# Kernel optimization log

Measured on AMD Instinct MI355X. Metric: run time of the kernel, lower is better.

The kernel has to match this reference:

```python
import jax, jax.numpy as jnp
import numpy as np

A = 5.0  # smoothness parameter


def setup_inputs() -> dict:
    key = jax.random.key(0)
    kx, kw = jax.random.split(key)
    x = jax.random.uniform(kx, (4096, 256), dtype=jnp.float32)
    weight = jax.random.uniform(kw, (256, 256), dtype=jnp.float32)
    return {"x": x, "weight": weight}


def reference(x, weight):
    # inner: [batch, in_features, out_features] broadcast elementwise max
    inner = jnp.maximum(x[..., None], weight[None])
    # smooth min over in_features (dim=-2): -(1/a) * logsumexp(-a * inner)
    smooth = -jax.nn.logsumexp(-A * inner, axis=-2) / A
    # hard min over same dim
    hard = jnp.min(inner, axis=-2)
    # straight-through estimator: forward value = hard, gradient flows via smooth
    return jax.lax.stop_gradient(hard - smooth) + smooth
```

## Files before the change

### kernel.cpp

```cpp
#include <hip/hip_runtime.h>


typedef _Float16 h2 __attribute__((ext_vector_type(2)));

union U4H { uint4 u; h2 h[4]; };

static __device__ __forceinline__ h2 pmin(h2 a, h2 b) {
#if __has_builtin(__builtin_elementwise_min)
    return __builtin_elementwise_min(a, b);
#else
    h2 d; asm("v_pk_min_f16 %0, %1, %2" : "=v"(d) : "v"(a), "v"(b)); return d;
#endif
}
static __device__ __forceinline__ h2 pmax(h2 a, h2 b) {
#if __has_builtin(__builtin_elementwise_max)
    return __builtin_elementwise_max(a, b);
#else
    h2 d; asm("v_pk_max_f16 %0, %1, %2" : "=v"(d) : "v"(a), "v"(b)); return d;
#endif
}

__global__ __launch_bounds__(256, 1)
void SmoothSTEMinMax_kernel(const float* __restrict__ x,
                            const float* __restrict__ w,
                            float* __restrict__ out) {
    __shared__ __align__(16) unsigned char smem[65536];
    unsigned char* xs = smem;
    unsigned char* ws = smem + 32768;

    const int t  = threadIdx.x;
    const int r0 = blockIdx.y * 64;
    const int c0 = blockIdx.x * 64;

    {
        const int i4 = t & 63;
        const int wv = t >> 6;
#pragma unroll
        for (int k = 0; k < 8; ++k) {
            const int rr = (k << 2) + wv;
            const float4 va = *reinterpret_cast<const float4*>(&x[(size_t)(r0 + rr)      * 256 + (i4 << 2)]);
            const float4 vb = *reinterpret_cast<const float4*>(&x[(size_t)(r0 + rr + 32) * 256 + (i4 << 2)]);
            U4H q;
            q.h[0] = h2{(_Float16)va.x, (_Float16)va.y};
            q.h[1] = h2{(_Float16)va.z, (_Float16)va.w};
            q.h[2] = h2{(_Float16)vb.x, (_Float16)vb.y};
            q.h[3] = h2{(_Float16)vb.z, (_Float16)vb.w};
            const int line = rr ^ (i4 & 31);
            *reinterpret_cast<uint4*>(xs + (i4 << 9) + (line << 4)) = q.u;
        }
    }

#pragma unroll
    for (int k = 0; k < 8; ++k) {
        const int flat = k * 256 + t;
        const int p  = flat >> 4;
        const int cq = flat & 15;
        const float4 va = *reinterpret_cast<const float4*>(&w[(size_t)(2 * p)     * 256 + c0 + (cq << 2)]);
        const float4 vb = *reinterpret_cast<const float4*>(&w[(size_t)(2 * p + 1) * 256 + c0 + (cq << 2)]);
        U4H q;
        q.h[0] = h2{(_Float16)va.x, (_Float16)vb.x};
        q.h[1] = h2{(_Float16)va.y, (_Float16)vb.y};
        q.h[2] = h2{(_Float16)va.z, (_Float16)vb.z};
        q.h[3] = h2{(_Float16)va.w, (_Float16)vb.w};
        *reinterpret_cast<uint4*>(ws + p * 256 + (cq << 4)) = q.u;
    }

    __syncthreads();

    const int tr = t >> 4;
    const int tc = t & 15;

    h2 acc[4][4];
    const h2 big = h2{(_Float16)65504.0f, (_Float16)65504.0f};
#pragma unroll
    for (int m = 0; m < 4; ++m)
#pragma unroll
        for (int n = 0; n < 4; ++n) acc[m][n] = big;

#pragma unroll 4
    for (int i4 = 0; i4 < 64; ++i4) {
        const unsigned char* xb = xs + (i4 << 9);
        const int kk = i4 & 31;
        U4H xu0, xu1, wqa, wqb;
        xu0.u = *reinterpret_cast<const uint4*>(xb + ((((tr << 1)    ) ^ kk) << 4));
        xu1.u = *reinterpret_cast<const uint4*>(xb + ((((tr << 1) | 1) ^ kk) << 4));
        const unsigned char* wb = ws + (i4 << 9);
        wqa.u = *reinterpret_cast<const uint4*>(wb       + (tc << 4));
        wqb.u = *reinterpret_cast<const uint4*>(wb + 256 + (tc << 4));

        h2 xA[4] = { xu0.h[0], xu0.h[2], xu1.h[0], xu1.h[2] };
        h2 xB[4] = { xu0.h[1], xu0.h[3], xu1.h[1], xu1.h[3] };
        h2 wA[4] = { wqa.h[0], wqa.h[1], wqa.h[2], wqa.h[3] };
        h2 wB[4] = { wqb.h[0], wqb.h[1], wqb.h[2], wqb.h[3] };

#pragma unroll
        for (int m = 0; m < 4; ++m)
#pragma unroll
            for (int n = 0; n < 4; ++n) {
                acc[m][n] = pmin(acc[m][n], pmax(xA[m], wA[n]));
                acc[m][n] = pmin(acc[m][n], pmax(xB[m], wB[n]));
            }
    }

    const int rowm[4] = { 2 * tr, 2 * tr + 32, 2 * tr + 1, 2 * tr + 33 };
#pragma unroll
    for (int m = 0; m < 4; ++m) {
        float4 o;
        o.x = fminf((float)acc[m][0].x, (float)acc[m][0].y);
        o.y = fminf((float)acc[m][1].x, (float)acc[m][1].y);
        o.z = fminf((float)acc[m][2].x, (float)acc[m][2].y);
        o.w = fminf((float)acc[m][3].x, (float)acc[m][3].y);
        *reinterpret_cast<float4*>(&out[(size_t)(r0 + rowm[m]) * 256 + c0 + (tc << 2)]) = o;
    }
}

extern "C" void kernel_launch(void* const* d_in, const int* in_sizes, int n_in,
                              void* d_out, int out_size, void* d_ws, size_t ws_size,
                              hipStream_t stream) {
    const float* x = (const float*)d_in[0];
    const float* w = (const float*)d_in[1];
    float* out = (float*)d_out;

    const int batch = in_sizes[0] / 256;
    dim3 grid(256 / 64, batch / 64);
    dim3 block(256);
    hipLaunchKernelGGL(SmoothSTEMinMax_kernel, grid, block, 0, stream, x, w, out);
}
```

Baseline: 19.96 us.

## Use 1024-thread blocks with one output column per thread

Each block now runs 1024 threads instead of 256, and each thread computes 4 outputs (one column, four rows) rather than a 4x4 tile. The weight staging is relaid out so each thread reads an 8-byte slice per k-step, and outputs are written as scalar stores. The aim is more latency hiding and more parallel waves per block, at the cost of less register-level reuse: there are more shared-memory loads per min/max operation and stores are no longer vectorized.

```diff
diff --git a/kernel.cpp b/kernel.cpp
--- a/kernel.cpp
+++ b/kernel.cpp
@@ -4,6 +4,7 @@
 typedef _Float16 h2 __attribute__((ext_vector_type(2)));
 
 union U4H { uint4 u; h2 h[4]; };
+union U2H { uint2 u; h2 h[2]; };
 
 static __device__ __forceinline__ h2 pmin(h2 a, h2 b) {
 #if __has_builtin(__builtin_elementwise_min)
@@ -20,7 +21,7 @@
 #endif
 }
 
-__global__ __launch_bounds__(256, 1)
+__global__ __launch_bounds__(1024, 4)
 void SmoothSTEMinMax_kernel(const float* __restrict__ x,
                             const float* __restrict__ w,
                             float* __restrict__ out) {
@@ -36,8 +37,8 @@
         const int i4 = t & 63;
         const int wv = t >> 6;
 #pragma unroll
-        for (int k = 0; k < 8; ++k) {
-            const int rr = (k << 2) + wv;
+        for (int k = 0; k < 2; ++k) {
+            const int rr = (k << 4) + wv;
             const float4 va = *reinterpret_cast<const float4*>(&x[(size_t)(r0 + rr)      * 256 + (i4 << 2)]);
             const float4 vb = *reinterpret_cast<const float4*>(&x[(size_t)(r0 + rr + 32) * 256 + (i4 << 2)]);
             U4H q;
@@ -51,67 +52,54 @@
     }
 
 #pragma unroll
-    for (int k = 0; k < 8; ++k) {
-        const int flat = k * 256 + t;
-        const int p  = flat >> 4;
-        const int cq = flat & 15;
-        const float4 va = *reinterpret_cast<const float4*>(&w[(size_t)(2 * p)     * 256 + c0 + (cq << 2)]);
-        const float4 vb = *reinterpret_cast<const float4*>(&w[(size_t)(2 * p + 1) * 256 + c0 + (cq << 2)]);
-        U4H q;
-        q.h[0] = h2{(_Float16)va.x, (_Float16)vb.x};
-        q.h[1] = h2{(_Float16)va.y, (_Float16)vb.y};
-        q.h[2] = h2{(_Float16)va.z, (_Float16)vb.z};
-        q.h[3] = h2{(_Float16)va.w, (_Float16)vb.w};
-        *reinterpret_cast<uint4*>(ws + p * 256 + (cq << 4)) = q.u;
+    for (int k = 0; k < 4; ++k) {
+        const int flat = (k << 10) + t;
+        const int i4  = (flat >> 6) & 63;
+        const int col = flat & 63;
+        const float f0 = w[(size_t)((i4 << 2) + 0) * 256 + c0 + col];
+        const float f1 = w[(size_t)((i4 << 2) + 1) * 256 + c0 + col];
+        const float f2 = w[(size_t)((i4 << 2) + 2) * 256 + c0 + col];
+        const float f3 = w[(size_t)((i4 << 2) + 3) * 256 + c0 + col];
+        U2H q;
+        q.h[0] = h2{(_Float16)f0, (_Float16)f1};
+        q.h[1] = h2{(_Float16)f2, (_Float16)f3};
+        *reinterpret_cast<uint2*>(ws + (i4 << 9) + (col << 3)) = q.u;
     }
 
     __syncthreads();
 
-    const int tr = t >> 4;
-    const int tc = t & 15;
+    const int tr = t >> 6;
+    const int tc = t & 63;
 
-    h2 acc[4][4];
+    h2 acc0, acc1, acc2, acc3;
     const h2 big = h2{(_Float16)65504.0f, (_Float16)65504.0f};
-#pragma unroll
-    for (int m = 0; m < 4; ++m)
-#pragma unroll
-        for (int n = 0; n < 4; ++n) acc[m][n] = big;
+    acc0 = acc1 = acc2 = acc3 = big;
 
 #pragma unroll 4
     for (int i4 = 0; i4 < 64; ++i4) {
         const unsigned char* xb = xs + (i4 << 9);
         const int kk = i4 & 31;
-        U4H xu0, xu1, wqa, wqb;
+        U4H xu0, xu1; U2H wq;
         xu0.u = *reinterpret_cast<const uint4*>(xb + ((((tr << 1)    ) ^ kk) << 4));
         xu1.u = *reinterpret_cast<const uint4*>(xb + ((((tr << 1) | 1) ^ kk) << 4));
-        const unsigned char* wb = ws + (i4 << 9);
-        wqa.u = *reinterpret_cast<const uint4*>(wb       + (tc << 4));
-        wqb.u = *reinterpret_cast<const uint4*>(wb + 256 + (tc << 4));
+        wq.u  = *reinterpret_cast<const uint2*>(ws + (i4 << 9) + (tc << 3));
 
-        h2 xA[4] = { xu0.h[0], xu0.h[2], xu1.h[0], xu1.h[2] };
-        h2 xB[4] = { xu0.h[1], xu0.h[3], xu1.h[1], xu1.h[3] };
-        h2 wA[4] = { wqa.h[0], wqa.h[1], wqa.h[2], wqa.h[3] };
-        h2 wB[4] = { wqb.h[0], wqb.h[1], wqb.h[2], wqb.h[3] };
-
-#pragma unroll
-        for (int m = 0; m < 4; ++m)
-#pragma unroll
-            for (int n = 0; n < 4; ++n) {
-                acc[m][n] = pmin(acc[m][n], pmax(xA[m], wA[n]));
-                acc[m][n] = pmin(acc[m][n], pmax(xB[m], wB[n]));
-            }
+        const h2 wA = wq.h[0], wB = wq.h[1];
+        acc0 = pmin(acc0, pmax(xu0.h[0], wA)); acc0 = pmin(acc0, pmax(xu0.h[1], wB));
+        acc1 = pmin(acc1, pmax(xu0.h[2], wA)); acc1 = pmin(acc1, pmax(xu0.h[3], wB));
+        acc2 = pmin(acc2, pmax(xu1.h[0], wA)); acc2 = pmin(acc2, pmax(xu1.h[1], wB));
+        acc3 = pmin(acc3, pmax(xu1.h[2], wA)); acc3 = pmin(acc3, pmax(xu1.h[3], wB));
     }
 
     const int rowm[4] = { 2 * tr, 2 * tr + 32, 2 * tr + 1, 2 * tr + 33 };
-#pragma unroll
-    for (int m = 0; m < 4; ++m) {
-        float4 o;
-        o.x = fminf((float)acc[m][0].x, (float)acc[m][0].y);
-        o.y = fminf((float)acc[m][1].x, (float)acc[m][1].y);
-        o.z = fminf((float)acc[m][2].x, (float)acc[m][2].y);
-        o.w = fminf((float)acc[m][3].x, (float)acc[m][3].y);
-        *reinterpret_cast<float4*>(&out[(size_t)(r0 + rowm[m]) * 256 + c0 + (tc << 2)]) = o;
-    }
+    const float o0 = fminf((float)acc0.x, (float)acc0.y);
+    const float o1 = fminf((float)acc1.x, (float)acc1.y);
+    const float o2 = fminf((float)acc2.x, (float)acc2.y);
+    const float o3 = fminf((float)acc3.x, (float)acc3.y);
+    out[(size_t)(r0 + rowm[0]) * 256 + c0 + tc] = o0;
+    out[(size_t)(r0 + rowm[1]) * 256 + c0 + tc] = o1;
+    out[(size_t)(r0 + rowm[2]) * 256 + c0 + tc] = o2;
+    out[(size_t)(r0 + rowm[3]) * 256 + c0 + tc] = o3;
 }
 
 extern "C" void kernel_launch(void* const* d_in, const int* in_sizes, int n_in,
@@ -123,6 +111,6 @@
 
     const int batch = in_sizes[0] / 256;
     dim3 grid(256 / 64, batch / 64);
-    dim3 block(256);
+    dim3 block(1024);
     hipLaunchKernelGGL(SmoothSTEMinMax_kernel, grid, block, 0, stream, x, w, out);
 }
```

Result: slower. 23.46 us (+17.5%).
